# Kernel optimization log

Hardware: AMD Instinct MI355X
Metric: run time of the kernel (lower is better)

The kernel has to match this reference:

```python
import jax, jax.numpy as jnp
import numpy as np

N, D, K = 16384, 256, 4096  # encoded vectors, embedding_dim, codebook_size


def setup_inputs() -> dict:
    key = jax.random.key(0)
    k_ze, k_cb = jax.random.split(key)
    ze = jax.random.normal(k_ze, (N, D), dtype=jnp.float32)
    codebook = jax.random.normal(k_cb, (K, D), dtype=jnp.float32)
    return {"ze": ze, "codebook": codebook}


def reference(ze, codebook):
    # Pairwise squared distances: ||ze||^2 + ||e||^2 - 2 ze e^T  -> [N, K]
    sq_norm = (
        jnp.sum(ze ** 2, axis=-1, keepdims=True)
        + jnp.sum(codebook ** 2, axis=1)
        - 2.0 * jnp.matmul(ze, codebook.T)
    )
    indices = jnp.argmin(sq_norm, axis=-1)            # [N]
    zq = jnp.take(codebook, indices, axis=0)          # [N, D] gather

    # VQ losses (stop-gradient mirrors .detach())
    vq_e_loss = jnp.mean((zq - jax.lax.stop_gradient(ze)) ** 2)
    vq_commit_loss = jnp.mean((jax.lax.stop_gradient(zq) - ze) ** 2)

    # perplexity: probs[i] = count_i / 10 (faithful to original, incl. /10)
    counts = jnp.zeros((K,), dtype=jnp.float32).at[indices].add(1.0)
    probs = counts / 10.0
    perplexity = jnp.exp(-jnp.sum(probs * jnp.log(probs + 1e-10)))

    return indices, zq, vq_e_loss, vq_commit_loss, perplexity
```

## Files before the change

### kernel.cpp

```cpp
#include <hip/hip_runtime.h>
#include <math.h>

#define N_TOT 16384
#define DIM   256
#define KCB   4096

typedef __attribute__((ext_vector_type(8)))  short s8v;
typedef __attribute__((ext_vector_type(16))) float f16v;

#define PK_OFF   32832
#define CBF_OFF  163904
#define WS_NEED  4358208ull
#define ZERO_W   36880

__device__ __forceinline__ void gload16(const void* g, void* l) {
  __builtin_amdgcn_global_load_lds(
      (const __attribute__((address_space(1))) unsigned int*)g,
      (__attribute__((address_space(3))) unsigned int*)l, 16, 0, 0);
}

__global__ __launch_bounds__(256)
void cb_prep_k(const float* __restrict__ cb, float* __restrict__ ws) {
  const int t = threadIdx.x, tile = blockIdx.x;
  for (int i = tile * 256 + t; i < ZERO_W; i += 128 * 256) ws[KCB + i] = 0.0f;

  const int col = t >> 3, j = t & 7;
  const int c0  = tile * 32;
  ushort* tb = (ushort*)((char*)ws + CBF_OFF) + (size_t)tile * 16384;
  const float* src = cb + (size_t)(c0 + col) * DIM;
  float s = 0.0f;
  #pragma unroll
  for (int ks = 0; ks < 16; ++ks) {
    #pragma unroll
    for (int kh = 0; kh < 2; ++kh) {
      float x = src[ks * 16 + kh * 8 + j];
      s += x * x;
      unsigned xb = __float_as_uint(x);
      unsigned hb = xb & 0xFFFF0000u;
      float lf = x - __uint_as_float(hb);
      tb[ks * 512 + kh * 256 + t]        = (ushort)(xb >> 16);
      tb[8192 + ks * 512 + kh * 256 + t] = (ushort)(__float_as_uint(lf) >> 16);
    }
  }
  s += __shfl_down(s, 4, 8);
  s += __shfl_down(s, 2, 8);
  s += __shfl_down(s, 1, 8);
  if (j == 0) ws[c0 + col] = s;
}

#define AP 260

__global__ __launch_bounds__(512, 2)
void vq_mfma_k(const float* __restrict__ ze, float* __restrict__ ws) {
  __shared__ __align__(16) char ldsU[3 * 32768 + 4096];
  float* sCbn = (float*)(ldsU + 3 * 32768);

  const int t    = threadIdx.x;
  const int lane = t & 63;
  const int w    = t >> 6;
  const int ln31 = lane & 31;
  const int hl   = lane >> 5;
  const int mb   = blockIdx.x >> 2;
  const int cq   = blockIdx.x & 3;
  const int m0   = mb * 256;

  const float* cbn = ws;
  unsigned long long* pk = (unsigned long long*)((char*)ws + PK_OFF);
  const char* cbF = (const char*)ws + CBF_OFF;

  s8v ah[16], al[16];
  float* Af = (float*)ldsU;
  for (int c = 0; c < 4; ++c) {
    __syncthreads();
    {
      int r  = t >> 3;
      int f0 = t & 7;
      const float* src = ze + (size_t)(m0 + c * 64 + r) * DIM;
      #pragma unroll
      for (int i = 0; i < 8; ++i) {
        int f = f0 + 8 * i;
        *(float4*)&Af[r * AP + f * 4] = *(const float4*)(src + f * 4);
      }
    }
    __syncthreads();
    if ((w >> 1) == c) {
      int rl = (w & 1) * 32 + ln31;
      #pragma unroll
      for (int ks = 0; ks < 16; ++ks) {
        float4 x0 = *(const float4*)&Af[rl * AP + ks * 16 + hl * 8];
        float4 x1 = *(const float4*)&Af[rl * AP + ks * 16 + hl * 8 + 4];
        float xs[8] = {x0.x, x0.y, x0.z, x0.w, x1.x, x1.y, x1.z, x1.w};
        #pragma unroll
        for (int j = 0; j < 8; ++j) {
          unsigned xb = __float_as_uint(xs[j]);
          unsigned hb = xb & 0xFFFF0000u;
          float lf = xs[j] - __uint_as_float(hb);
          ah[ks][j] = (short)(xb >> 16);
          al[ks][j] = (short)(__float_as_uint(lf) >> 16);
        }
      }
    }
  }
  if (t < 512) {
    sCbn[t]       = cbn[cq * 1024 + t];
    sCbn[t + 512] = cbn[cq * 1024 + 512 + t];
  }
  __syncthreads();

  const char* qbase = cbF + (size_t)cq * 32 * 32768;

  #pragma unroll
  for (int pt = 0; pt < 2; ++pt) {
    const char* g = qbase + (size_t)pt * 32768 + (size_t)w * 4096 + (size_t)lane * 16;
    char* lp = ldsU + pt * 32768 + w * 4096;
    #pragma unroll
    for (int ii = 0; ii < 4; ++ii) gload16(g + ii * 1024, lp + ii * 1024);
  }

  float best[16];
  int   bidx[16];
  #pragma unroll
  for (int r = 0; r < 16; ++r) { best[r] = -1e30f; bidx[r] = 0; }

  const char* bR = ldsU;
  char*       bW = ldsU + 2 * 32768;

  #pragma unroll 1
  for (int tt = 0; tt < 32; ++tt) {
    if (tt == 31) { asm volatile("s_waitcnt vmcnt(0)" ::: "memory"); }
    else          { asm volatile("s_waitcnt vmcnt(4)" ::: "memory"); }
    __builtin_amdgcn_s_barrier();
    __builtin_amdgcn_sched_barrier(0);

    if (tt + 2 < 32) {
      const char* g = qbase + (size_t)(tt + 2) * 32768 + (size_t)w * 4096 + (size_t)lane * 16;
      char* lp = bW + w * 4096;
      #pragma unroll
      for (int ii = 0; ii < 4; ++ii) gload16(g + ii * 1024, lp + ii * 1024);
    }

    const int   c0      = cq * 1024 + tt * 32;
    const float half_cv = 0.5f * sCbn[tt * 32 + ln31];
    const char* bc      = bR;

    f16v hh, xx;
    #pragma unroll
    for (int r = 0; r < 16; ++r) { hh[r] = 0.0f; xx[r] = 0.0f; }

    __builtin_amdgcn_s_setprio(1);
    #pragma unroll
    for (int ks = 0; ks < 16; ++ks) {
      s8v bh = *(const s8v*)(bc + ks * 1024 + lane * 16);
      s8v bl = *(const s8v*)(bc + 16384 + ks * 1024 + lane * 16);
      hh = __builtin_amdgcn_mfma_f32_32x32x16_bf16(ah[ks], bh, hh, 0, 0, 0);
      xx = __builtin_amdgcn_mfma_f32_32x32x16_bf16(ah[ks], bl, xx, 0, 0, 0);
      xx = __builtin_amdgcn_mfma_f32_32x32x16_bf16(al[ks], bh, xx, 0, 0, 0);
    }
    __builtin_amdgcn_s_setprio(0);

    #pragma unroll
    for (int r = 0; r < 16; ++r) {
      float s = hh[r] + xx[r] - half_cv;
      if (s > best[r]) { best[r] = s; bidx[r] = c0 + ln31; }
    }

    bR += 32768; if (bR == ldsU + 3 * 32768) bR = ldsU;
    bW += 32768; if (bW == ldsU + 3 * 32768) bW = ldsU;
  }

  #pragma unroll
  for (int r = 0; r < 16; ++r) {
    float s = best[r];
    int   c = bidx[r];
    #pragma unroll
    for (int mk = 1; mk < 32; mk <<= 1) {
      float os = __shfl_xor(s, mk, 64);
      int   oc = __shfl_xor(c, mk, 64);
      if (os > s || (os == s && oc < c)) { s = os; c = oc; }
    }
    if (ln31 == 0) {
      int row = m0 + w * 32 + (r & 3) + 8 * (r >> 2) + 4 * hl;
      unsigned u = __float_as_uint(s);
      unsigned enc = (u & 0x80000000u) ? ~u : (u | 0x80000000u);
      unsigned long long p = ((unsigned long long)enc << 32) | (unsigned)(KCB - 1 - c);
      atomicMax(&pk[row], p);
    }
  }
}

__global__ __launch_bounds__(256)
void gather_k(const float* __restrict__ ze, const float* __restrict__ cb,
              float* __restrict__ ws, float* __restrict__ out) {
  __shared__ int sIdx[64];
  const int t  = threadIdx.x;
  const int m0 = blockIdx.x * 64;
  float* counts   = ws + KCB;
  float* loss_sum = ws + 2 * KCB;
  const unsigned long long* pk = (const unsigned long long*)((const char*)ws + PK_OFF);

  if (t < 64) {
    unsigned long long p = pk[m0 + t];
    int col = KCB - 1 - (int)(unsigned)(p & 0xFFFFFFFFull);
    out[m0 + t] = (float)col;
    sIdx[t] = col;
    atomicAdd(&counts[col], 1.0f);
  }
  __syncthreads();

  float* out_zq = out + N_TOT;
  const int w = t >> 6, ln = t & 63;
  float lsum = 0.0f;
  #pragma unroll
  for (int p = 0; p < 16; ++p) {
    int r = w + 4 * p;
    float4 cvv = *(const float4*)(cb + (size_t)sIdx[r] * DIM + ln * 4);
    float4 zv  = *(const float4*)(ze + (size_t)(m0 + r) * DIM + ln * 4);
    *(float4*)(out_zq + (size_t)(m0 + r) * DIM + ln * 4) = cvv;
    float dx = cvv.x - zv.x, dy = cvv.y - zv.y, dz = cvv.z - zv.z, dw = cvv.w - zv.w;
    lsum += dx * dx + dy * dy + dz * dz + dw * dw;
  }
  #pragma unroll
  for (int off = 32; off > 0; off >>= 1) lsum += __shfl_down(lsum, off, 64);
  if (ln == 0) atomicAdd(loss_sum, lsum);
}

__global__ void zero_ws_k(float* __restrict__ ws, int nw) {
  int i = blockIdx.x * 256 + threadIdx.x;
  if (i < nw) ws[KCB + i] = 0.0f;
}

__global__ void cbnorm_k(const float* __restrict__ cb, float* __restrict__ ws) {
  int row  = blockIdx.x * 4 + (threadIdx.x >> 6);
  int lane = threadIdx.x & 63;
  float4 v = *(const float4*)(cb + (size_t)row * DIM + lane * 4);
  float s = v.x*v.x + v.y*v.y + v.z*v.z + v.w*v.w;
  #pragma unroll
  for (int off = 32; off > 0; off >>= 1) s += __shfl_down(s, off, 64);
  if (lane == 0) ws[row] = s;
}

#define FBM 32
#define FBN 64
#define FBD 128
__global__ __launch_bounds__(256, 4)
void vq_main_k(const float* __restrict__ ze, const float* __restrict__ cb,
               float* __restrict__ ws, float* __restrict__ out) {
  __shared__ float As[FBM * FBD];
  __shared__ float Bs[FBN * FBD];
  __shared__ float red_d[FBM * 16];
  __shared__ int   red_i[FBM * 16];
  __shared__ int   sIdx[FBM];

  const int t  = threadIdx.x;
  const int tx = t & 15;
  const int ty = t >> 4;
  const int m0 = blockIdx.x * FBM;

  const float* cbn = ws;
  float* counts    = ws + KCB;
  float* loss_sum  = ws + 2 * KCB;

  float best0 = 1e30f, best1 = 1e30f;
  int   bidx0 = 0,     bidx1 = 0;
  const int sA = ty & 7;
  const int sB = tx & 7;

  for (int kt = 0; kt < KCB / FBN; ++kt) {
    float cbnj[4];
    #pragma unroll
    for (int j = 0; j < 4; ++j) cbnj[j] = cbn[kt * FBN + tx + 16 * j];
    float acc[2][4];
    #pragma unroll
    for (int i = 0; i < 2; ++i)
      #pragma unroll
      for (int j = 0; j < 4; ++j) acc[i][j] = 0.0f;

    for (int dc = 0; dc < DIM / FBD; ++dc) {
      __syncthreads();
      {
        int c  = t & 31;
        int rb = t >> 5;
        #pragma unroll
        for (int p = 0; p < 4; ++p) {
          int r = rb + 8 * p;
          float4 v = *(const float4*)(ze + (size_t)(m0 + r) * DIM + dc * FBD + c * 4);
          *(float4*)&As[r * FBD + ((c ^ (r & 7)) << 2)] = v;
        }
        #pragma unroll
        for (int p = 0; p < 8; ++p) {
          int r = rb + 8 * p;
          float4 v = *(const float4*)(cb + (size_t)(kt * FBN + r) * DIM + dc * FBD + c * 4);
          *(float4*)&Bs[r * FBD + ((c ^ (r & 7)) << 2)] = v;
        }
      }
      __syncthreads();
      #pragma unroll 8
      for (int ds = 0; ds < FBD / 4; ++ds) {
        float4 a0 = *(const float4*)&As[ty * FBD + ((ds ^ sA) << 2)];
        float4 a1 = *(const float4*)&As[(ty + 16) * FBD + ((ds ^ sA) << 2)];
        float4 b[4];
        #pragma unroll
        for (int j = 0; j < 4; ++j)
          b[j] = *(const float4*)&Bs[(tx + 16 * j) * FBD + ((ds ^ sB) << 2)];
        #pragma unroll
        for (int j = 0; j < 4; ++j) {
          acc[0][j] = fmaf(a0.x, b[j].x, acc[0][j]);
          acc[0][j] = fmaf(a0.y, b[j].y, acc[0][j]);
          acc[0][j] = fmaf(a0.z, b[j].z, acc[0][j]);
          acc[0][j] = fmaf(a0.w, b[j].w, acc[0][j]);
          acc[1][j] = fmaf(a1.x, b[j].x, acc[1][j]);
          acc[1][j] = fmaf(a1.y, b[j].y, acc[1][j]);
          acc[1][j] = fmaf(a1.z, b[j].z, acc[1][j]);
          acc[1][j] = fmaf(a1.w, b[j].w, acc[1][j]);
        }
      }
    }
    #pragma unroll
    for (int j = 0; j < 4; ++j) {
      int kg = kt * FBN + tx + 16 * j;
      float d0 = cbnj[j] - 2.0f * acc[0][j];
      float d1 = cbnj[j] - 2.0f * acc[1][j];
      if (d0 < best0) { best0 = d0; bidx0 = kg; }
      if (d1 < best1) { best1 = d1; bidx1 = kg; }
    }
  }

  __syncthreads();
  red_d[ty * 16 + tx] = best0;        red_i[ty * 16 + tx] = bidx0;
  red_d[(ty + 16) * 16 + tx] = best1; red_i[(ty + 16) * 16 + tx] = bidx1;
  __syncthreads();

  if (t < FBM) {
    float bd = red_d[t * 16]; int bi = red_i[t * 16];
    #pragma unroll
    for (int q = 1; q < 16; ++q) {
      float d = red_d[t * 16 + q]; int i2 = red_i[t * 16 + q];
      if (d < bd || (d == bd && i2 < bi)) { bd = d; bi = i2; }
    }
    out[m0 + t] = (float)bi;
    sIdx[t] = bi;
    atomicAdd(&counts[bi], 1.0f);
  }
  __syncthreads();

  float* out_zq = out + N_TOT;
  const int wv = t >> 6, ln = t & 63;
  float lsum = 0.0f;
  #pragma unroll
  for (int p = 0; p < 8; ++p) {
    int r = wv + 4 * p;
    float4 cvv = *(const float4*)(cb + (size_t)sIdx[r] * DIM + ln * 4);
    float4 zv  = *(const float4*)(ze + (size_t)(m0 + r) * DIM + ln * 4);
    *(float4*)(out_zq + (size_t)(m0 + r) * DIM + ln * 4) = cvv;
    float dx = cvv.x - zv.x, dy = cvv.y - zv.y, dz = cvv.z - zv.z, dw = cvv.w - zv.w;
    lsum += dx*dx + dy*dy + dz*dz + dw*dw;
  }
  #pragma unroll
  for (int off = 32; off > 0; off >>= 1) lsum += __shfl_down(lsum, off, 64);
  if (ln == 0) atomicAdd(loss_sum, lsum);
}

__global__ void finalize_k(const float* __restrict__ ws, float* __restrict__ out) {
  __shared__ float red[256];
  int t = threadIdx.x;
  const float* counts = ws + KCB;
  float s = 0.0f;
  for (int k = t; k < KCB; k += 256) {
    float p = counts[k] * 0.1f;
    s += p * logf(p + 1e-10f);
  }
  red[t] = s;
  __syncthreads();
  for (int q = 128; q > 0; q >>= 1) { if (t < q) red[t] += red[t + q]; __syncthreads(); }
  if (t == 0) {
    float loss = ws[2 * KCB] / (float)((size_t)N_TOT * DIM);
    float* o = out + N_TOT + (size_t)N_TOT * DIM;
    o[0] = loss;
    o[1] = loss;
    o[2] = expf(-red[0]);
  }
}

extern "C" void kernel_launch(void* const* d_in, const int* in_sizes, int n_in,
                              void* d_out, int out_size, void* d_ws, size_t ws_size,
                              hipStream_t stream) {
  const float* ze = (const float*)d_in[0];
  const float* cb = (const float*)d_in[1];
  float* out = (float*)d_out;
  float* ws  = (float*)d_ws;

  if (ws_size >= WS_NEED) {
    cb_prep_k<<<128, 256, 0, stream>>>(cb, ws);
    vq_mfma_k<<<256, 512, 0, stream>>>(ze, ws);
    gather_k<<<N_TOT / 64, 256, 0, stream>>>(ze, cb, ws, out);
  } else {
    zero_ws_k<<<(KCB + 1 + 255) / 256, 256, 0, stream>>>(ws, KCB + 1);
    cbnorm_k<<<KCB / 4, 256, 0, stream>>>(cb, ws);
    vq_main_k<<<N_TOT / FBM, 256, 0, stream>>>(ze, cb, ws, out);
  }
  finalize_k<<<1, 256, 0, stream>>>(ws, out);
}
```

Measured before the change: 194.5 us.

## Give each wave two 32-row A tiles to reuse codebook B fragments

The block shrinks from 8 to 4 waves, and each wave now holds two 32-row blocks of ze as bf16 hi/lo fragments. Each codebook fragment read from LDS therefore feeds six MFMAs instead of three, halving LDS read traffic per MFMA. The B fragments are register-prefetched one k-step ahead, and the codebook-norm term is folded into the accumulator initialisation. The cost is roughly double the register use for A fragments and best/idx state, fewer waves to hide latency, and each wave issuing twice as many global-to-LDS loads.

```diff
diff --git a/kernel.cpp b/kernel.cpp
--- a/kernel.cpp
+++ b/kernel.cpp
@@ -50,7 +50,7 @@
 
 #define AP 260
 
-__global__ __launch_bounds__(512, 2)
+__global__ __launch_bounds__(256, 1)
 void vq_mfma_k(const float* __restrict__ ze, float* __restrict__ ws) {
   __shared__ __align__(16) char ldsU[3 * 32768 + 4096];
   float* sCbn = (float*)(ldsU + 3 * 32768);
@@ -68,14 +68,14 @@
   unsigned long long* pk = (unsigned long long*)((char*)ws + PK_OFF);
   const char* cbF = (const char*)ws + CBF_OFF;
 
-  s8v ah[16], al[16];
+  s8v ah[2][16], al[2][16];
   float* Af = (float*)ldsU;
-  for (int c = 0; c < 4; ++c) {
+  for (int c = 0; c < 8; ++c) {
     __syncthreads();
     {
       int r  = t >> 3;
       int f0 = t & 7;
-      const float* src = ze + (size_t)(m0 + c * 64 + r) * DIM;
+      const float* src = ze + (size_t)(m0 + c * 32 + r) * DIM;
       #pragma unroll
       for (int i = 0; i < 8; ++i) {
         int f = f0 + 8 * i;
@@ -83,44 +83,43 @@
       }
     }
     __syncthreads();
-    if ((w >> 1) == c) {
-      int rl = (w & 1) * 32 + ln31;
+    if (w == (c >> 1)) {
+      const int rb = c & 1;
+      const int rl = ln31;
       #pragma unroll
       for (int ks = 0; ks < 16; ++ks) {
-        float4 x0 = *(const float4*)&Af[rl * AP + ks * 16 + hl * 8];
-        float4 x1 = *(const float4*)&Af[rl * AP + ks * 16 + hl * 8 + 4];
-        float xs[8] = {x0.x, x0.y, x0.z, x0.w, x1.x, x1.y, x1.z, x1.w};
+        float4 q0 = *(const float4*)&Af[rl * AP + ks * 16 + hl * 8];
+        float4 q1 = *(const float4*)&Af[rl * AP + ks * 16 + hl * 8 + 4];
+        float xs[8] = {q0.x, q0.y, q0.z, q0.w, q1.x, q1.y, q1.z, q1.w};
         #pragma unroll
         for (int j = 0; j < 8; ++j) {
           unsigned xb = __float_as_uint(xs[j]);
           unsigned hb = xb & 0xFFFF0000u;
           float lf = xs[j] - __uint_as_float(hb);
-          ah[ks][j] = (short)(xb >> 16);
-          al[ks][j] = (short)(__float_as_uint(lf) >> 16);
+          ah[rb][ks][j] = (short)(xb >> 16);
+          al[rb][ks][j] = (short)(__float_as_uint(lf) >> 16);
         }
       }
     }
   }
-  if (t < 512) {
-    sCbn[t]       = cbn[cq * 1024 + t];
-    sCbn[t + 512] = cbn[cq * 1024 + 512 + t];
-  }
+  #pragma unroll
+  for (int i = 0; i < 4; ++i) sCbn[t + 256 * i] = cbn[cq * 1024 + t + 256 * i];
   __syncthreads();
 
   const char* qbase = cbF + (size_t)cq * 32 * 32768;
 
   #pragma unroll
   for (int pt = 0; pt < 2; ++pt) {
-    const char* g = qbase + (size_t)pt * 32768 + (size_t)w * 4096 + (size_t)lane * 16;
-    char* lp = ldsU + pt * 32768 + w * 4096;
-    #pragma unroll
-    for (int ii = 0; ii < 4; ++ii) gload16(g + ii * 1024, lp + ii * 1024);
-  }
-
-  float best[16];
-  int   bidx[16];
-  #pragma unroll
-  for (int r = 0; r < 16; ++r) { best[r] = -1e30f; bidx[r] = 0; }
+    const char* g = qbase + (size_t)pt * 32768 + (size_t)w * 8192 + (size_t)lane * 16;
+    char* lp = ldsU + pt * 32768 + w * 8192;
+    #pragma unroll
+    for (int ii = 0; ii < 8; ++ii) gload16(g + ii * 1024, lp + ii * 1024);
+  }
+
+  float best[32];
+  int   bidx[32];
+  #pragma unroll
+  for (int r = 0; r < 32; ++r) { best[r] = -1e30f; bidx[r] = 0; }
 
   const char* bR = ldsU;
   char*       bW = ldsU + 2 * 32768;
@@ -128,40 +127,49 @@
   #pragma unroll 1
   for (int tt = 0; tt < 32; ++tt) {
     if (tt == 31) { asm volatile("s_waitcnt vmcnt(0)" ::: "memory"); }
-    else          { asm volatile("s_waitcnt vmcnt(4)" ::: "memory"); }
+    else          { asm volatile("s_waitcnt vmcnt(8)" ::: "memory"); }
     __builtin_amdgcn_s_barrier();
     __builtin_amdgcn_sched_barrier(0);
 
     if (tt + 2 < 32) {
-      const char* g = qbase + (size_t)(tt + 2) * 32768 + (size_t)w * 4096 + (size_t)lane * 16;
-      char* lp = bW + w * 4096;
+      const char* g = qbase + (size_t)(tt + 2) * 32768 + (size_t)w * 8192 + (size_t)lane * 16;
+      char* lp = bW + w * 8192;
       #pragma unroll
-      for (int ii = 0; ii < 4; ++ii) gload16(g + ii * 1024, lp + ii * 1024);
+      for (int ii = 0; ii < 8; ++ii) gload16(g + ii * 1024, lp + ii * 1024);
     }
 
     const int   c0      = cq * 1024 + tt * 32;
     const float half_cv = 0.5f * sCbn[tt * 32 + ln31];
-    const char* bc      = bR;
-
-    f16v hh, xx;
-    #pragma unroll
-    for (int r = 0; r < 16; ++r) { hh[r] = 0.0f; xx[r] = 0.0f; }
-
+    const s8v*  bp      = (const s8v*)(bR + (size_t)lane * 16);
+
+    f16v h0, x0, h1, x1;
+    #pragma unroll
+    for (int r = 0; r < 16; ++r) {
+      h0[r] = -half_cv; h1[r] = -half_cv; x0[r] = 0.0f; x1[r] = 0.0f;
+    }
+
+    s8v cbh = bp[0], cbl = bp[1024];
     __builtin_amdgcn_s_setprio(1);
     #pragma unroll
     for (int ks = 0; ks < 16; ++ks) {
-      s8v bh = *(const s8v*)(bc + ks * 1024 + lane * 16);
-      s8v bl = *(const s8v*)(bc + 16384 + ks * 1024 + lane * 16);
-      hh = __builtin_amdgcn_mfma_f32_32x32x16_bf16(ah[ks], bh, hh, 0, 0, 0);
-      xx = __builtin_amdgcn_mfma_f32_32x32x16_bf16(ah[ks], bl, xx, 0, 0, 0);
-      xx = __builtin_amdgcn_mfma_f32_32x32x16_bf16(al[ks], bh, xx, 0, 0, 0);
+      s8v nbh = cbh, nbl = cbl;
+      if (ks < 15) { nbh = bp[(ks + 1) * 64]; nbl = bp[1024 + (ks + 1) * 64]; }
+      h0 = __builtin_amdgcn_mfma_f32_32x32x16_bf16(ah[0][ks], cbh, h0, 0, 0, 0);
+      h1 = __builtin_amdgcn_mfma_f32_32x32x16_bf16(ah[1][ks], cbh, h1, 0, 0, 0);
+      x0 = __builtin_amdgcn_mfma_f32_32x32x16_bf16(ah[0][ks], cbl, x0, 0, 0, 0);
+      x1 = __builtin_amdgcn_mfma_f32_32x32x16_bf16(ah[1][ks], cbl, x1, 0, 0, 0);
+      x0 = __builtin_amdgcn_mfma_f32_32x32x16_bf16(al[0][ks], cbh, x0, 0, 0, 0);
+      x1 = __builtin_amdgcn_mfma_f32_32x32x16_bf16(al[1][ks], cbh, x1, 0, 0, 0);
+      cbh = nbh; cbl = nbl;
     }
     __builtin_amdgcn_s_setprio(0);
 
     #pragma unroll
     for (int r = 0; r < 16; ++r) {
-      float s = hh[r] + xx[r] - half_cv;
-      if (s > best[r]) { best[r] = s; bidx[r] = c0 + ln31; }
+      float s0 = h0[r] + x0[r];
+      if (s0 > best[r])      { best[r]      = s0; bidx[r]      = c0 + ln31; }
+      float s1 = h1[r] + x1[r];
+      if (s1 > best[16 + r]) { best[16 + r] = s1; bidx[16 + r] = c0 + ln31; }
     }
 
     bR += 32768; if (bR == ldsU + 3 * 32768) bR = ldsU;
@@ -169,7 +177,7 @@
   }
 
   #pragma unroll
-  for (int r = 0; r < 16; ++r) {
+  for (int r = 0; r < 32; ++r) {
     float s = best[r];
     int   c = bidx[r];
     #pragma unroll
@@ -179,7 +187,8 @@
       if (os > s || (os == s && oc < c)) { s = os; c = oc; }
     }
     if (ln31 == 0) {
-      int row = m0 + w * 32 + (r & 3) + 8 * (r >> 2) + 4 * hl;
+      int rb = r >> 4, rr = r & 15;
+      int row = m0 + w * 64 + rb * 32 + (rr & 3) + 8 * (rr >> 2) + 4 * hl;
       unsigned u = __float_as_uint(s);
       unsigned enc = (u & 0x80000000u) ? ~u : (u | 0x80000000u);
       unsigned long long p = ((unsigned long long)enc << 32) | (unsigned)(KCB - 1 - c);
@@ -391,7 +400,7 @@
 
   if (ws_size >= WS_NEED) {
     cb_prep_k<<<128, 256, 0, stream>>>(cb, ws);
-    vq_mfma_k<<<256, 512, 0, stream>>>(ze, ws);
+    vq_mfma_k<<<256, 256, 0, stream>>>(ze, ws);
     gather_k<<<N_TOT / 64, 256, 0, stream>>>(ze, cb, ws, out);
   } else {
     zero_ws_k<<<(KCB + 1 + 255) / 256, 256, 0, stream>>>(ws, KCB + 1);
```

Measured after the change: 232.6 us. 19.6% more time.
